# Optimization experiments

Measured on AMD Instinct MI355X. Metric: run time of the kernel, lower is better.

The kernel has to match this reference:

```python
import jax, jax.numpy as jnp
import numpy as np
from jax import lax

K = 15            # k_neighbors
EPS = 1e-8
N, D = 8192, 512


def _knn(emb, k):
    # pairwise euclidean distances via gram trick (torch.cdist p=2 equivalent)
    sq = jnp.sum(emb * emb, axis=1)                      # [N]
    d2 = sq[:, None] + sq[None, :] - 2.0 * (emb @ emb.T)  # [N, N]
    d = jnp.where(d2 > 0, jnp.sqrt(jnp.maximum(d2, 1e-24)), 0.0)
    neg_d, idx = lax.top_k(-d, k + 1)                    # smallest k+1 (incl. self)
    return -neg_d[:, 1:], idx[:, 1:]                     # drop self: [N,k], [N,k]


def _local_density(knn_dists):
    return 1.0 / (knn_dists.mean(axis=1) + EPS)          # [N]


def _angular_signature(emb, knn_idx, k):
    nb = emb[knn_idx]                                    # [N, k, D] gather
    v = nb - emb[:, None, :]                             # [N, k, D]
    v = v / jnp.maximum(jnp.linalg.norm(v, axis=2, keepdims=True), 1e-12)
    cos = jnp.einsum('nkd,nld->nkl', v, v)               # [N, k, k]
    iu0, iu1 = np.triu_indices(k, 1)                     # static upper-triangle mask
    return cos[:, iu0, iu1]                              # [N, k*(k-1)/2]


def setup_inputs() -> dict:
    key = jax.random.key(0)
    k1, k2 = jax.random.split(key)
    embeddings = jax.random.normal(k1, (N, D), dtype=jnp.float32)
    ref_embeddings = jax.random.normal(k2, (N, D), dtype=jnp.float32)
    return {"embeddings": embeddings, "ref_embeddings": ref_embeddings}


def reference(embeddings, ref_embeddings):
    k = K
    # reference geometry is a detached buffer (set_reference under no_grad)
    ref = lax.stop_gradient(ref_embeddings)
    ref_dists, ref_idx = _knn(ref, k)
    ref_density = _local_density(ref_dists)
    ref_angular = _angular_signature(ref, ref_idx, k)

    curr_dists, curr_idx = _knn(embeddings, k)

    # 1) normalized distance-distribution loss
    curr_dn = curr_dists / (curr_dists.mean(axis=1, keepdims=True) + EPS)
    ref_dn = ref_dists / (ref_dists.mean(axis=1, keepdims=True) + EPS)
    total = jnp.mean((curr_dn - ref_dn) ** 2)

    # 2) density preservation loss (use_density=True)
    curr_density = _local_density(curr_dists)
    cden = curr_density / (curr_density.mean() + EPS)
    rden = ref_density / (ref_density.mean() + EPS)
    total = total + 0.5 * jnp.mean((cden - rden) ** 2)

    # 3) angular structure loss (use_angular=True)
    curr_angular = _angular_signature(embeddings, curr_idx, k)
    total = total + 0.5 * jnp.mean((curr_angular - ref_angular) ** 2)
    return total
```

## Files before the change

kernel.cpp:

```cpp
#include <hip/hip_runtime.h>

#define N 8192
#define D 512
#define KNN 15
#define SC 8
#define NC 16
#define SPLITS 8
#define NCAND 32
#define NPAIR 105
#define EPSF 1e-8f

#define RB 32
#define CB 64
#define KB 32

#define INF __int_as_float(0x7f800000)

typedef __attribute__((ext_vector_type(4))) float f32x4;
typedef __attribute__((ext_vector_type(8))) short s16x8;
typedef __attribute__((ext_vector_type(8))) unsigned short u16x8;
typedef unsigned long long u64;

typedef const unsigned int __attribute__((address_space(1)))* gp_t;
typedef unsigned int __attribute__((address_space(3)))* lp_t;

__device__ __forceinline__ void gl_lds16(const void* g, void* l) {
  __builtin_amdgcn_global_load_lds((gp_t)g, (lp_t)l, 16, 0, 0);
}

__device__ __forceinline__ unsigned short bf16_rne(float x) {
  unsigned int u = __float_as_uint(x);
  return (unsigned short)((u + 0x7fffu + ((u >> 16) & 1u)) >> 16);
}

#define VMCNT4 asm volatile("s_waitcnt vmcnt(4)" ::: "memory")
#define VMCNT0 asm volatile("s_waitcnt vmcnt(0)" ::: "memory")
#define LGKM0  asm volatile("s_waitcnt lgkmcnt(0)" ::: "memory")
#define CFENCE asm volatile("" ::: "memory")

__global__ __launch_bounds__(256)
void k_sqnorm(const float* __restrict__ A, const float* __restrict__ B,
              float* __restrict__ sq)
{
  int tid = threadIdx.x;
  int lane = tid & 63;
  int row = blockIdx.x * 4 + (tid >> 6);
  const float* src = (row < N) ? (A + (size_t)row * D)
                               : (B + (size_t)(row - N) * D);
  const float4* s4 = (const float4*)src + lane * 2;
  float4 x0 = s4[0], x1 = s4[1];
  float s = x0.x*x0.x + x0.y*x0.y + x0.z*x0.z + x0.w*x0.w
          + x1.x*x1.x + x1.y*x1.y + x1.z*x1.z + x1.w*x1.w;
#pragma unroll
  for (int o = 32; o; o >>= 1) s += __shfl_xor(s, o);
  if (lane == 0) sq[row] = s;
}

__global__ __launch_bounds__(256)
void k_split_hi(const float* __restrict__ A, const float* __restrict__ B,
                unsigned short* __restrict__ hi)
{
  size_t t = (size_t)blockIdx.x * 256 + threadIdx.x;
  size_t base = t * 8;
  const float* src = (base < (size_t)N * D) ? (A + base) : (B + (base - (size_t)N * D));
  float4 x0 = ((const float4*)src)[0];
  float4 x1 = ((const float4*)src)[1];
  float xs[8] = {x0.x, x0.y, x0.z, x0.w, x1.x, x1.y, x1.z, x1.w};
  u16x8 hv;
#pragma unroll
  for (int j = 0; j < 8; ++j) hv[j] = bf16_rne(xs[j]);
  *(u16x8*)(hi + base) = hv;
}

__global__ __launch_bounds__(256, 4)
void k_knn1(const unsigned short* __restrict__ hi,
            const float* __restrict__ sqall,
            unsigned* __restrict__ pk)
{
  __shared__ __align__(16) char smem[40960];
  float* Dt = (float*)smem;
  unsigned* SK = (unsigned*)smem;

  const int tid = threadIdx.x;
  const int lane = tid & 63, w = tid >> 6;
  const int wr = w >> 1, wc = w & 1;
  const int fr = lane & 15, fq = lane >> 4;
  const int sgx = fq ^ ((fr >> 1) & 3);

  const int rb = blockIdx.x, split = blockIdx.y, which = blockIdx.z;
  const int row0 = rb * 128;
  const int c0 = split * 1024;
  const unsigned short* Hi = hi + (size_t)which * N * D;
  const float* sq = sqall + which * N;

  const int rr = tid >> 2, sseg = tid & 3;
  const int ssg = sseg ^ ((rr >> 1) & 3);
  const unsigned short* pAh = Hi + (size_t)(row0 + rr) * D + ssg * 8;
  const unsigned short* pBh = Hi + (size_t)(c0 + rr) * D + ssg * 8;

  auto stage = [&](int sel) {
    char* d = smem + (sel << 14) + (w << 10);
    gl_lds16(pAh, d);
    gl_lds16(pAh + 32768, d + 4096);
    gl_lds16(pBh, d + 8192);
    gl_lds16(pBh + 32768, d + 12288);
    pAh += 32; pBh += 32;
  };

  const int srow = tid >> 1, ssub = tid & 1;
  unsigned tv[SC];
#pragma unroll
  for (int j = 0; j < SC; ++j) tv[j] = 0xFFFFFFFFu;

  float sqr[4][4];
#pragma unroll
  for (int m = 0; m < 4; ++m)
#pragma unroll
    for (int j = 0; j < 4; ++j)
      sqr[m][j] = sq[row0 + wr * 64 + m * 16 + fq * 4 + j];

#pragma unroll 1
  for (int t = 0; t < 8; ++t) {
    const int ct = c0 + t * 128;
    float sqc[4];
#pragma unroll
    for (int n = 0; n < 4; ++n) sqc[n] = sq[ct + wc * 64 + n * 16 + fr];

    f32x4 acc[4][4];
#pragma unroll
    for (int m = 0; m < 4; ++m)
#pragma unroll
      for (int n = 0; n < 4; ++n) acc[m][n] = (f32x4){0.f, 0.f, 0.f, 0.f};

    stage(0);
    int cur = 0;
#pragma unroll 1
    for (int kt = 0; kt < 16; ++kt) {
      if (kt < 15) {
        stage(cur ^ 1);
        VMCNT4;
      } else {
        VMCNT0;
      }
      __builtin_amdgcn_s_barrier();
      CFENCE;

      const short* Sb = (const short*)(smem + (cur << 14));
      s16x8 ah[4], bh[4];
#pragma unroll
      for (int m = 0; m < 4; ++m)
        ah[m] = *(const s16x8*)(Sb + (wr * 64 + m * 16 + fr) * 32 + sgx * 8);
#pragma unroll
      for (int n = 0; n < 4; ++n)
        bh[n] = *(const s16x8*)(Sb + 4096 + (wc * 64 + n * 16 + fr) * 32 + sgx * 8);
#pragma unroll
      for (int m = 0; m < 4; ++m)
#pragma unroll
        for (int n = 0; n < 4; ++n)
          acc[m][n] = __builtin_amdgcn_mfma_f32_16x16x32_bf16(ah[m], bh[n], acc[m][n], 0, 0, 0);

      LGKM0;
      __builtin_amdgcn_s_barrier();
      CFENCE;
      cur ^= 1;
    }
    pAh -= 512; pBh += 65024;

#pragma unroll 1
    for (int h = 0; h < 2; ++h) {
      if (wc == h) {
#pragma unroll
        for (int m = 0; m < 4; ++m)
#pragma unroll
          for (int n = 0; n < 4; ++n) {
            const int cl = n * 16 + fr;
            const int gcol = ct + h * 64 + cl;
            const int rbase = wr * 64 + m * 16 + fq * 4;
#pragma unroll
            for (int j = 0; j < 4; ++j) {
              float d2 = fmaf(-2.0f, acc[m][n][j], sqr[m][j] + sqc[n]);
              if (row0 + rbase + j == gcol) d2 = INF;
              Dt[(rbase + j) * 68 + cl] = d2;
            }
          }
      }
      __syncthreads();
      {
        unsigned kth = tv[SC - 1];
        const int lb = t * 128 + h * 64 + ssub * 32;
#pragma unroll 1
        for (int g = 0; g < 8; ++g) {
          const f32x4 dv = *(const f32x4*)&Dt[srow * 68 + ssub * 32 + g * 4];
#pragma unroll
          for (int i = 0; i < 4; ++i) {
            const float d2c = fmaxf(dv[i], 0.0f);
            unsigned key = (__float_as_uint(d2c) & ~1023u) | (unsigned)(lb + g * 4 + i);
            if (key < kth) {
#pragma unroll
              for (int j = 0; j < SC; ++j) {
                const unsigned lo = min(tv[j], key);
                key = max(tv[j], key);
                tv[j] = lo;
              }
              kth = tv[SC - 1];
            }
          }
        }
      }
      __syncthreads();
    }
  }

#pragma unroll
  for (int j = 0; j < SC; ++j) SK[srow * 16 + ssub * 8 + j] = tv[j];
  __syncthreads();
  if (tid < 128) {
    const int grow = row0 + tid;
    const size_t pb = (((size_t)which * SPLITS + split) * N + grow) * NC;
    int p0 = 0, p1 = 0;
#pragma unroll
    for (int j = 0; j < NC; ++j) {
      const unsigned a = (p0 < SC) ? SK[tid * 16 + p0] : 0xFFFFFFFFu;
      const unsigned b = (p1 < SC) ? SK[tid * 16 + 8 + p1] : 0xFFFFFFFFu;
      const bool ta = a <= b;
      pk[pb + j] = ta ? a : b;
      if (ta) ++p0; else ++p1;
    }
  }
}

__global__ __launch_bounds__(256)
void k_cand(const unsigned* __restrict__ pk, int* __restrict__ cidx)
{
  const int flat = blockIdx.x * 256 + threadIdx.x;
  const int which = flat >> 13, row = flat & (N - 1);
  const size_t b0 = (((size_t)which * SPLITS + 0) * N + row) * NC;
  const size_t b1 = (((size_t)which * SPLITS + 1) * N + row) * NC;
  const size_t b2 = (((size_t)which * SPLITS + 2) * N + row) * NC;
  const size_t b3 = (((size_t)which * SPLITS + 3) * N + row) * NC;
  const size_t b4 = (((size_t)which * SPLITS + 4) * N + row) * NC;
  const size_t b5 = (((size_t)which * SPLITS + 5) * N + row) * NC;
  const size_t b6 = (((size_t)which * SPLITS + 6) * N + row) * NC;
  const size_t b7 = (((size_t)which * SPLITS + 7) * N + row) * NC;
  unsigned v0 = pk[b0], v1 = pk[b1], v2 = pk[b2], v3 = pk[b3];
  unsigned v4 = pk[b4], v5 = pk[b5], v6 = pk[b6], v7 = pk[b7];
  int p0 = 0, p1 = 0, p2 = 0, p3 = 0, p4 = 0, p5 = 0, p6 = 0, p7 = 0;
  const size_t ob = ((size_t)which * N + row) * NCAND;
#pragma unroll 1
  for (int j = 0; j < NCAND; ++j) {
    const bool a01 = v0 <= v1; const unsigned m01 = a01 ? v0 : v1; const int s01 = a01 ? 0 : 1;
    const bool a23 = v2 <= v3; const unsigned m23 = a23 ? v2 : v3; const int s23 = a23 ? 2 : 3;
    const bool a45 = v4 <= v5; const unsigned m45 = a45 ? v4 : v5; const int s45 = a45 ? 4 : 5;
    const bool a67 = v6 <= v7; const unsigned m67 = a67 ? v6 : v7; const int s67 = a67 ? 6 : 7;
    const bool qA = m01 <= m23; const unsigned mA = qA ? m01 : m23; const int sA = qA ? s01 : s23;
    const bool qB = m45 <= m67; const unsigned mB = qB ? m45 : m67; const int sB = qB ? s45 : s67;
    const bool qf = mA <= mB;  const unsigned m = qf ? mA : mB;    const int sw = qf ? sA : sB;
    cidx[ob + j] = (sw << 10) | (int)(m & 1023u);
    if      (sw == 0) { ++p0; v0 = (p0 < NC) ? pk[b0 + p0] : 0xFFFFFFFFu; }
    else if (sw == 1) { ++p1; v1 = (p1 < NC) ? pk[b1 + p1] : 0xFFFFFFFFu; }
    else if (sw == 2) { ++p2; v2 = (p2 < NC) ? pk[b2 + p2] : 0xFFFFFFFFu; }
    else if (sw == 3) { ++p3; v3 = (p3 < NC) ? pk[b3 + p3] : 0xFFFFFFFFu; }
    else if (sw == 4) { ++p4; v4 = (p4 < NC) ? pk[b4 + p4] : 0xFFFFFFFFu; }
    else if (sw == 5) { ++p5; v5 = (p5 < NC) ? pk[b5 + p5] : 0xFFFFFFFFu; }
    else if (sw == 6) { ++p6; v6 = (p6 < NC) ? pk[b6 + p6] : 0xFFFFFFFFu; }
    else              { ++p7; v7 = (p7 < NC) ? pk[b7 + p7] : 0xFFFFFFFFu; }
  }
}

__global__ __launch_bounds__(256)
void k_rescore(const float* __restrict__ emb, const float* __restrict__ ref,
               const float* __restrict__ sqall, const int* __restrict__ cidx,
               float* __restrict__ knnd, int* __restrict__ knni)
{
  const int tid = threadIdx.x;
  const int lane = tid & 63, w = tid >> 6;
  const int flat = blockIdx.x * 4 + w;
  const int which = flat >> 13, row = flat & (N - 1);
  const float* E = which ? ref : emb;
  const float* sq = sqall + which * N;
  const int* cb = cidx + ((size_t)which * N + row) * NCAND;

  const float4* orow = (const float4*)(E + (size_t)row * D) + lane * 2;
  const float4 o0 = orow[0], o1 = orow[1];
  const float sqr = sq[row];

  u64 mykey = ~0ull;
#pragma unroll 4
  for (int c = 0; c < NCAND; ++c) {
    const int cl = cb[c];
    const float4* crow = (const float4*)(E + (size_t)cl * D) + lane * 2;
    const float4 c0 = crow[0], c1 = crow[1];
    float s = o0.x*c0.x + o0.y*c0.y + o0.z*c0.z + o0.w*c0.w
            + o1.x*c1.x + o1.y*c1.y + o1.z*c1.z + o1.w*c1.w;
#pragma unroll
    for (int o = 32; o; o >>= 1) s += __shfl_xor(s, o);
    float d2 = fmaf(-2.0f, s, sqr + sq[cl]);
    d2 = fmaxf(d2, 0.0f);
    const u64 key = ((u64)__float_as_uint(d2) << 32) | (unsigned)cl;
    if (lane == c) mykey = key;
  }

#pragma unroll
  for (int k = 2; k <= 64; k <<= 1) {
#pragma unroll
    for (int j = k >> 1; j > 0; j >>= 1) {
      const u64 o = __shfl_xor(mykey, j);
      const bool up = ((lane & k) == 0);
      const bool lower = ((lane & j) == 0);
      const u64 mn = (mykey < o) ? mykey : o;
      const u64 mx = (mykey < o) ? o : mykey;
      mykey = (lower == up) ? mn : mx;
    }
  }

  const size_t ob = ((size_t)which * N + row) * KNN;
  if (lane < KNN) {
    const float d2v = __uint_as_float((unsigned)(mykey >> 32));
    knnd[ob + lane] = (d2v > 0.f) ? sqrtf(fmaxf(d2v, 1e-24f)) : 0.f;
    knni[ob + lane] = (int)(mykey & 0xffffffffu);
  }
}

__global__ __launch_bounds__(256)
void k_knn_fb(const float* __restrict__ Ecur, const float* __restrict__ Eref,
              const float* __restrict__ sqall,
              float* __restrict__ knnd, int* __restrict__ knni)
{
  const int which = blockIdx.y;
  const float* E = which ? Eref : Ecur;
  const float* sq = sqall + which * N;
  float* outd = knnd + (size_t)which * N * KNN;
  int* outi = knni + (size_t)which * N * KNN;
  const int row0 = blockIdx.x * RB;

  __shared__ float As[RB][KB + 1];
  __shared__ float Bs[KB][CB + 4];
  __shared__ float Dtf[RB][CB + 1];
  __shared__ float topv[RB][KNN];
  __shared__ int topi[RB][KNN];

  const int tid = threadIdx.x;
  const int tx = tid & 15, ty = tid >> 4;

  if (tid < RB) {
#pragma unroll
    for (int j = 0; j < KNN; ++j) { topv[tid][j] = INF; topi[tid][j] = -1; }
  }

  for (int ct = 0; ct < N; ct += CB) {
    float acc[2][4] = {{0.f,0.f,0.f,0.f},{0.f,0.f,0.f,0.f}};
    for (int kt = 0; kt < D; kt += KB) {
      __syncthreads();
      {
        int r = tid >> 3, c4 = (tid & 7) << 2;
        const float4 v = *(const float4*)&E[(size_t)(row0 + r) * D + kt + c4];
        As[r][c4+0] = v.x; As[r][c4+1] = v.y; As[r][c4+2] = v.z; As[r][c4+3] = v.w;
      }
      {
        int k = tid & 31, cbase = tid >> 5;
#pragma unroll
        for (int i = 0; i < 8; ++i) {
          int c = cbase + (i << 3);
          Bs[k][c] = E[(size_t)(ct + c) * D + kt + k];
        }
      }
      __syncthreads();
#pragma unroll
      for (int k = 0; k < KB; ++k) {
        float a0 = As[2*ty + 0][k], a1 = As[2*ty + 1][k];
        float4 b = *(const float4*)&Bs[k][tx << 2];
        acc[0][0] = fmaf(a0, b.x, acc[0][0]); acc[0][1] = fmaf(a0, b.y, acc[0][1]);
        acc[0][2] = fmaf(a0, b.z, acc[0][2]); acc[0][3] = fmaf(a0, b.w, acc[0][3]);
        acc[1][0] = fmaf(a1, b.x, acc[1][0]); acc[1][1] = fmaf(a1, b.y, acc[1][1]);
        acc[1][2] = fmaf(a1, b.z, acc[1][2]); acc[1][3] = fmaf(a1, b.w, acc[1][3]);
      }
    }
    {
      float sr0 = sq[row0 + 2*ty + 0], sr1 = sq[row0 + 2*ty + 1];
#pragma unroll
      for (int c = 0; c < 4; ++c) {
        int gc = ct + (tx << 2) + c;
        float scv = sq[gc];
        float d20 = sr0 + scv - 2.0f * acc[0][c];
        float d21 = sr1 + scv - 2.0f * acc[1][c];
        float d0 = (d20 > 0.0f) ? sqrtf(fmaxf(d20, 1e-24f)) : 0.0f;
        float d1 = (d21 > 0.0f) ? sqrtf(fmaxf(d21, 1e-24f)) : 0.0f;
        if (gc == row0 + 2*ty + 0) d0 = INF;
        if (gc == row0 + 2*ty + 1) d1 = INF;
        Dtf[2*ty + 0][(tx << 2) + c] = d0;
        Dtf[2*ty + 1][(tx << 2) + c] = d1;
      }
    }
    __syncthreads();
    if (tid < RB) {
      float kth = topv[tid][KNN-1];
      for (int c = 0; c < CB; ++c) {
        float d = Dtf[tid][c];
        if (d < kth) {
          int gi = ct + c;
          int j = KNN - 1;
          while (j > 0 && topv[tid][j-1] > d) {
            topv[tid][j] = topv[tid][j-1]; topi[tid][j] = topi[tid][j-1]; --j;
          }
          topv[tid][j] = d; topi[tid][j] = gi;
          kth = topv[tid][KNN-1];
        }
      }
    }
    __syncthreads();
  }
  if (tid < RB) {
    int gr = row0 + tid;
#pragma unroll
    for (int j = 0; j < KNN; ++j) {
      outd[(size_t)gr * KNN + j] = topv[tid][j];
      outi[(size_t)gr * KNN + j] = topi[tid][j];
    }
  }
}

__global__ __launch_bounds__(256)
void k_ang3(const float* __restrict__ Ecur, const float* __restrict__ Eref,
            const int* __restrict__ knni, float* __restrict__ angpart)
{
  __shared__ __align__(16) short Vb[16][520];
  __shared__ float Gp[4][256];
  __shared__ float G[256];
  __shared__ float invn[16];
  __shared__ float cref[NPAIR];
  __shared__ float red2[256];

  const int i = blockIdx.x;
  const int tid = threadIdx.x;
  const int lane = tid & 63;
  const int w = tid >> 6;
  const int base = lane * 8;

  float acc = 0.f;

#pragma unroll 1
  for (int pass = 0; pass < 2; ++pass) {
    const float* E = pass ? Ecur : Eref;
    const int* idx = knni + ((size_t)(pass ? 0 : 1) * N + i) * KNN;

    const float4* er = (const float4*)(E + (size_t)i * D) + lane * 2;
    const float4 e0 = er[0], e1 = er[1];

#pragma unroll 1
    for (int j = w; j < 16; j += 4) {
      u16x8 hv;
      if (j < 15) {
        const float* src = E + (size_t)idx[j] * D;
        const float4 x0 = *(const float4*)(src + base);
        const float4 x1 = *(const float4*)(src + base + 4);
        const float dd[8] = {x0.x-e0.x, x0.y-e0.y, x0.z-e0.z, x0.w-e0.w,
                             x1.x-e1.x, x1.y-e1.y, x1.z-e1.z, x1.w-e1.w};
#pragma unroll
        for (int q = 0; q < 8; ++q) hv[q] = bf16_rne(dd[q]);
      } else {
#pragma unroll
        for (int q = 0; q < 8; ++q) hv[q] = 0;
      }
      *(u16x8*)&Vb[j][base] = hv;
    }
    __syncthreads();

    {
      const int r = lane & 15, fq = lane >> 4;
      f32x4 g = (f32x4){0.f, 0.f, 0.f, 0.f};
#pragma unroll
      for (int s = 0; s < 4; ++s) {
        const s16x8 f = *(const s16x8*)&Vb[r][w * 128 + s * 32 + fq * 8];
        g = __builtin_amdgcn_mfma_f32_16x16x32_bf16(f, f, g, 0, 0, 0);
      }
#pragma unroll
      for (int r2 = 0; r2 < 4; ++r2)
        Gp[w][(fq * 4 + r2) * 16 + r] = g[r2];
    }
    __syncthreads();

    G[tid] = Gp[0][tid] + Gp[1][tid] + Gp[2][tid] + Gp[3][tid];
    __syncthreads();
    if (tid < 16) invn[tid] = 1.0f / fmaxf(sqrtf(G[tid * 17]), 1e-12f);
    __syncthreads();

    if (tid < NPAIR) {
      int a = 0, q = tid, rem = KNN - 1;
      while (q >= rem) { q -= rem; ++a; --rem; }
      const int b = a + 1 + q;
      const float cosv = G[a * 16 + b] * invn[a] * invn[b];
      if (pass == 0) cref[tid] = cosv;
      else { const float dd = cosv - cref[tid]; acc = dd * dd; }
    }
    __syncthreads();
  }

  red2[tid] = acc;
  __syncthreads();
  for (int o = 128; o; o >>= 1) {
    if (tid < o) red2[tid] += red2[tid + o];
    __syncthreads();
  }
  if (tid == 0) angpart[i] = red2[0];
}

__global__ __launch_bounds__(256)
void k_stats(const float* __restrict__ knnd, float* __restrict__ dens,
             float* __restrict__ loss1part)
{
  __shared__ float red[256];
  int n = blockIdx.x * 256 + threadIdx.x;
  const float* dc = knnd + (size_t)n * KNN;
  const float* dr = knnd + (size_t)(N + n) * KNN;
  float mc = 0.f, mr = 0.f;
#pragma unroll
  for (int j = 0; j < KNN; ++j) { mc += dc[j]; mr += dr[j]; }
  mc *= (1.0f / KNN); mr *= (1.0f / KNN);
  float ic = 1.0f / (mc + EPSF);
  float ir = 1.0f / (mr + EPSF);
  float s = 0.f;
#pragma unroll
  for (int j = 0; j < KNN; ++j) {
    float t = dc[j] * ic - dr[j] * ir;
    s = fmaf(t, t, s);
  }
  dens[n] = ic;
  dens[N + n] = ir;
  red[threadIdx.x] = s;
  __syncthreads();
  for (int o = 128; o; o >>= 1) {
    if (threadIdx.x < o) red[threadIdx.x] += red[threadIdx.x + o];
    __syncthreads();
  }
  if (threadIdx.x == 0) loss1part[blockIdx.x] = red[0];
}

__global__ __launch_bounds__(256)
void k_final(const float* __restrict__ loss1part, const float* __restrict__ dens,
             const float* __restrict__ angpart, float* __restrict__ out)
{
  __shared__ float red[256];
  const int t = threadIdx.x;

  float sc = 0.f, sr = 0.f;
  for (int n = t; n < N; n += 256) { sc += dens[n]; sr += dens[N + n]; }
  red[t] = sc; __syncthreads();
  for (int o = 128; o; o >>= 1) { if (t < o) red[t] += red[t + o]; __syncthreads(); }
  float scm = red[0]; __syncthreads();
  red[t] = sr; __syncthreads();
  for (int o = 128; o; o >>= 1) { if (t < o) red[t] += red[t + o]; __syncthreads(); }
  float srm = red[0]; __syncthreads();

  float icm = 1.0f / (scm / (float)N + EPSF);
  float irm = 1.0f / (srm / (float)N + EPSF);

  float l2 = 0.f;
  for (int n = t; n < N; n += 256) {
    float dd = dens[n] * icm - dens[N + n] * irm;
    l2 = fmaf(dd, dd, l2);
  }
  red[t] = l2; __syncthreads();
  for (int o = 128; o; o >>= 1) { if (t < o) red[t] += red[t + o]; __syncthreads(); }
  float l2sum = red[0]; __syncthreads();

  float l1 = (t < 32) ? loss1part[t] : 0.f;
  red[t] = l1; __syncthreads();
  for (int o = 128; o; o >>= 1) { if (t < o) red[t] += red[t + o]; __syncthreads(); }
  float l1sum = red[0]; __syncthreads();

  float l3 = 0.f;
  for (int n = t; n < N; n += 256) l3 += angpart[n];
  red[t] = l3; __syncthreads();
  for (int o = 128; o; o >>= 1) { if (t < o) red[t] += red[t + o]; __syncthreads(); }
  float l3sum = red[0];

  if (t == 0) {
    out[0] = l1sum / (float)(N * KNN)
           + 0.5f * l2sum / (float)N
           + 0.5f * l3sum / (float)(N * NPAIR);
  }
}

extern "C" void kernel_launch(void* const* d_in, const int* in_sizes, int n_in,
                              void* d_out, int out_size, void* d_ws, size_t ws_size,
                              hipStream_t stream)
{
  const float* emb = (const float*)d_in[0];
  const float* ref = (const float*)d_in[1];
  float* out = (float*)d_out;
  char* ws = (char*)d_ws;

  const size_t off_sq = 0;
  const size_t off_hi = off_sq + (size_t)2 * N * 4;

  const size_t m_off_pk   = off_hi + (size_t)2 * N * D * 2;
  const size_t m_off_cidx = m_off_pk + (size_t)2 * SPLITS * N * NC * 4;
  const size_t m_off_knnd = m_off_cidx + (size_t)2 * N * NCAND * 4;
  const size_t m_off_knni = m_off_knnd + (size_t)2 * N * KNN * 4;
  const size_t m_off_angp = m_off_knni + (size_t)2 * N * KNN * 4;
  const size_t m_off_dens = m_off_angp + (size_t)N * 4;
  const size_t m_off_l1   = m_off_dens + (size_t)2 * N * 4;
  const size_t NEED       = m_off_l1 + 4096;

  float* sq = (float*)(ws + off_sq);
  float* knnd; int* knni; float* angpart; float* dens; float* l1part;

  k_sqnorm<<<(2 * N) / 4, 256, 0, stream>>>(emb, ref, sq);

  if (ws_size >= NEED) {
    unsigned short* hi = (unsigned short*)(ws + off_hi);
    unsigned* pk = (unsigned*)(ws + m_off_pk);
    int* cidx = (int*)(ws + m_off_cidx);
    knnd = (float*)(ws + m_off_knnd);
    knni = (int*)(ws + m_off_knni);
    angpart = (float*)(ws + m_off_angp);
    dens = (float*)(ws + m_off_dens);
    l1part = (float*)(ws + m_off_l1);

    k_split_hi<<<(2 * N * D / 8) / 256, 256, 0, stream>>>(emb, ref, hi);
    k_knn1<<<dim3(N / 128, SPLITS, 2), 256, 0, stream>>>(hi, sq, pk);
    k_cand<<<(2 * N) / 256, 256, 0, stream>>>(pk, cidx);
    k_rescore<<<(2 * N) / 4, 256, 0, stream>>>(emb, ref, sq, cidx, knnd, knni);
  } else {
    size_t o = off_hi;
    knnd = (float*)(ws + o); o += (size_t)2 * N * KNN * 4;
    knni = (int*)(ws + o);   o += (size_t)2 * N * KNN * 4;
    angpart = (float*)(ws + o); o += (size_t)N * 4;
    dens = (float*)(ws + o); o += (size_t)2 * N * 4;
    l1part = (float*)(ws + o);
    k_knn_fb<<<dim3(N / RB, 2), 256, 0, stream>>>(emb, ref, sq, knnd, knni);
  }

  k_ang3<<<N, 256, 0, stream>>>(emb, ref, knni, angpart);
  k_stats<<<N / 256, 256, 0, stream>>>(knnd, dens, l1part);
  k_final<<<1, 256, 0, stream>>>(l1part, dens, angpart, out);
}
```

Measured before the change: 396.1 us.

## Fuse prep kernels and merge candidate selection, rescoring, stats into angular kernel

Merges the squared-norm and bf16 split kernels into one pass over the inputs. The candidate-merge, rescore, stats and angular kernels become a single per-row tail kernel that bitonic-sorts the 128 partial keys inside a wavefront, rescores, and uses the neighbours directly from shared memory. The knn tile kernel now packs full 13-bit column indices into the keys when writing to shared memory, which drops low mantissa bits used in candidate ordering. This removes several launches and the intermediate candidate, distance and index buffers, but only two of the four waves do the merge and rescore work in the tail, and the fallback path for small workspaces is gone.

New measurement: 367.2 us. 1.08x faster.

```diff
diff --git a/kernel.cpp b/kernel.cpp
--- a/kernel.cpp
+++ b/kernel.cpp
@@ -10,13 +10,10 @@
 #define NPAIR 105
 #define EPSF 1e-8f
 
-#define RB 32
-#define CB 64
-#define KB 32
-
 #define INF __int_as_float(0x7f800000)
 
 typedef __attribute__((ext_vector_type(4))) float f32x4;
+typedef __attribute__((ext_vector_type(4))) unsigned u32x4;
 typedef __attribute__((ext_vector_type(8))) short s16x8;
 typedef __attribute__((ext_vector_type(8))) unsigned short u16x8;
 typedef unsigned long long u64;
@@ -39,37 +36,28 @@
 #define CFENCE asm volatile("" ::: "memory")
 
 __global__ __launch_bounds__(256)
-void k_sqnorm(const float* __restrict__ A, const float* __restrict__ B,
-              float* __restrict__ sq)
+void k_prep(const float* __restrict__ A, const float* __restrict__ B,
+            unsigned short* __restrict__ hi, float* __restrict__ sq)
 {
-  int tid = threadIdx.x;
-  int lane = tid & 63;
-  int row = blockIdx.x * 4 + (tid >> 6);
+  const int tid = threadIdx.x;
+  const int lane = tid & 63;
+  const int row = blockIdx.x * 4 + (tid >> 6);
   const float* src = (row < N) ? (A + (size_t)row * D)
                                : (B + (size_t)(row - N) * D);
   const float4* s4 = (const float4*)src + lane * 2;
-  float4 x0 = s4[0], x1 = s4[1];
-  float s = x0.x*x0.x + x0.y*x0.y + x0.z*x0.z + x0.w*x0.w
-          + x1.x*x1.x + x1.y*x1.y + x1.z*x1.z + x1.w*x1.w;
+  const float4 x0 = s4[0], x1 = s4[1];
+  const float xs[8] = {x0.x, x0.y, x0.z, x0.w, x1.x, x1.y, x1.z, x1.w};
+  u16x8 hv;
+  float s = 0.f;
+#pragma unroll
+  for (int j = 0; j < 8; ++j) {
+    hv[j] = bf16_rne(xs[j]);
+    s = fmaf(xs[j], xs[j], s);
+  }
+  *(u16x8*)(hi + (size_t)row * D + lane * 8) = hv;
 #pragma unroll
   for (int o = 32; o; o >>= 1) s += __shfl_xor(s, o);
   if (lane == 0) sq[row] = s;
-}
-
-__global__ __launch_bounds__(256)
-void k_split_hi(const float* __restrict__ A, const float* __restrict__ B,
-                unsigned short* __restrict__ hi)
-{
-  size_t t = (size_t)blockIdx.x * 256 + threadIdx.x;
-  size_t base = t * 8;
-  const float* src = (base < (size_t)N * D) ? (A + base) : (B + (base - (size_t)N * D));
-  float4 x0 = ((const float4*)src)[0];
-  float4 x1 = ((const float4*)src)[1];
-  float xs[8] = {x0.x, x0.y, x0.z, x0.w, x1.x, x1.y, x1.z, x1.w};
-  u16x8 hv;
-#pragma unroll
-  for (int j = 0; j < 8; ++j) hv[j] = bf16_rne(xs[j]);
-  *(u16x8*)(hi + base) = hv;
 }
 
 __global__ __launch_bounds__(256, 4)
@@ -78,7 +66,7 @@
             unsigned* __restrict__ pk)
 {
   __shared__ __align__(16) char smem[40960];
-  float* Dt = (float*)smem;
+  unsigned* DtU = (unsigned*)smem;
   unsigned* SK = (unsigned*)smem;
 
   const int tid = threadIdx.x;
@@ -178,23 +166,22 @@
             const int rbase = wr * 64 + m * 16 + fq * 4;
 #pragma unroll
             for (int j = 0; j < 4; ++j) {
-              float d2 = fmaf(-2.0f, acc[m][n][j], sqr[m][j] + sqc[n]);
-              if (row0 + rbase + j == gcol) d2 = INF;
-              Dt[(rbase + j) * 68 + cl] = d2;
+              const float d2 = fmaf(-2.0f, acc[m][n][j], sqr[m][j] + sqc[n]);
+              unsigned key = (__float_as_uint(fmaxf(d2, 0.f)) & ~8191u) | (unsigned)gcol;
+              if (row0 + rbase + j == gcol) key = 0xFFFFFFFFu;
+              DtU[(rbase + j) * 68 + cl] = key;
             }
           }
       }
       __syncthreads();
       {
         unsigned kth = tv[SC - 1];
-        const int lb = t * 128 + h * 64 + ssub * 32;
 #pragma unroll 1
         for (int g = 0; g < 8; ++g) {
-          const f32x4 dv = *(const f32x4*)&Dt[srow * 68 + ssub * 32 + g * 4];
+          const u32x4 dv = *(const u32x4*)&DtU[srow * 68 + ssub * 32 + g * 4];
 #pragma unroll
           for (int i = 0; i < 4; ++i) {
-            const float d2c = fmaxf(dv[i], 0.0f);
-            unsigned key = (__float_as_uint(d2c) & ~1023u) | (unsigned)(lb + g * 4 + i);
+            unsigned key = dv[i];
             if (key < kth) {
 #pragma unroll
               for (int j = 0; j < SC; ++j) {
@@ -230,198 +217,10 @@
 }
 
 __global__ __launch_bounds__(256)
-void k_cand(const unsigned* __restrict__ pk, int* __restrict__ cidx)
-{
-  const int flat = blockIdx.x * 256 + threadIdx.x;
-  const int which = flat >> 13, row = flat & (N - 1);
-  const size_t b0 = (((size_t)which * SPLITS + 0) * N + row) * NC;
-  const size_t b1 = (((size_t)which * SPLITS + 1) * N + row) * NC;
-  const size_t b2 = (((size_t)which * SPLITS + 2) * N + row) * NC;
-  const size_t b3 = (((size_t)which * SPLITS + 3) * N + row) * NC;
-  const size_t b4 = (((size_t)which * SPLITS + 4) * N + row) * NC;
-  const size_t b5 = (((size_t)which * SPLITS + 5) * N + row) * NC;
-  const size_t b6 = (((size_t)which * SPLITS + 6) * N + row) * NC;
-  const size_t b7 = (((size_t)which * SPLITS + 7) * N + row) * NC;
-  unsigned v0 = pk[b0], v1 = pk[b1], v2 = pk[b2], v3 = pk[b3];
-  unsigned v4 = pk[b4], v5 = pk[b5], v6 = pk[b6], v7 = pk[b7];
-  int p0 = 0, p1 = 0, p2 = 0, p3 = 0, p4 = 0, p5 = 0, p6 = 0, p7 = 0;
-  const size_t ob = ((size_t)which * N + row) * NCAND;
-#pragma unroll 1
-  for (int j = 0; j < NCAND; ++j) {
-    const bool a01 = v0 <= v1; const unsigned m01 = a01 ? v0 : v1; const int s01 = a01 ? 0 : 1;
-    const bool a23 = v2 <= v3; const unsigned m23 = a23 ? v2 : v3; const int s23 = a23 ? 2 : 3;
-    const bool a45 = v4 <= v5; const unsigned m45 = a45 ? v4 : v5; const int s45 = a45 ? 4 : 5;
-    const bool a67 = v6 <= v7; const unsigned m67 = a67 ? v6 : v7; const int s67 = a67 ? 6 : 7;
-    const bool qA = m01 <= m23; const unsigned mA = qA ? m01 : m23; const int sA = qA ? s01 : s23;
-    const bool qB = m45 <= m67; const unsigned mB = qB ? m45 : m67; const int sB = qB ? s45 : s67;
-    const bool qf = mA <= mB;  const unsigned m = qf ? mA : mB;    const int sw = qf ? sA : sB;
-    cidx[ob + j] = (sw << 10) | (int)(m & 1023u);
-    if      (sw == 0) { ++p0; v0 = (p0 < NC) ? pk[b0 + p0] : 0xFFFFFFFFu; }
-    else if (sw == 1) { ++p1; v1 = (p1 < NC) ? pk[b1 + p1] : 0xFFFFFFFFu; }
-    else if (sw == 2) { ++p2; v2 = (p2 < NC) ? pk[b2 + p2] : 0xFFFFFFFFu; }
-    else if (sw == 3) { ++p3; v3 = (p3 < NC) ? pk[b3 + p3] : 0xFFFFFFFFu; }
-    else if (sw == 4) { ++p4; v4 = (p4 < NC) ? pk[b4 + p4] : 0xFFFFFFFFu; }
-    else if (sw == 5) { ++p5; v5 = (p5 < NC) ? pk[b5 + p5] : 0xFFFFFFFFu; }
-    else if (sw == 6) { ++p6; v6 = (p6 < NC) ? pk[b6 + p6] : 0xFFFFFFFFu; }
-    else              { ++p7; v7 = (p7 < NC) ? pk[b7 + p7] : 0xFFFFFFFFu; }
-  }
-}
-
-__global__ __launch_bounds__(256)
-void k_rescore(const float* __restrict__ emb, const float* __restrict__ ref,
-               const float* __restrict__ sqall, const int* __restrict__ cidx,
-               float* __restrict__ knnd, int* __restrict__ knni)
-{
-  const int tid = threadIdx.x;
-  const int lane = tid & 63, w = tid >> 6;
-  const int flat = blockIdx.x * 4 + w;
-  const int which = flat >> 13, row = flat & (N - 1);
-  const float* E = which ? ref : emb;
-  const float* sq = sqall + which * N;
-  const int* cb = cidx + ((size_t)which * N + row) * NCAND;
-
-  const float4* orow = (const float4*)(E + (size_t)row * D) + lane * 2;
-  const float4 o0 = orow[0], o1 = orow[1];
-  const float sqr = sq[row];
-
-  u64 mykey = ~0ull;
-#pragma unroll 4
-  for (int c = 0; c < NCAND; ++c) {
-    const int cl = cb[c];
-    const float4* crow = (const float4*)(E + (size_t)cl * D) + lane * 2;
-    const float4 c0 = crow[0], c1 = crow[1];
-    float s = o0.x*c0.x + o0.y*c0.y + o0.z*c0.z + o0.w*c0.w
-            + o1.x*c1.x + o1.y*c1.y + o1.z*c1.z + o1.w*c1.w;
-#pragma unroll
-    for (int o = 32; o; o >>= 1) s += __shfl_xor(s, o);
-    float d2 = fmaf(-2.0f, s, sqr + sq[cl]);
-    d2 = fmaxf(d2, 0.0f);
-    const u64 key = ((u64)__float_as_uint(d2) << 32) | (unsigned)cl;
-    if (lane == c) mykey = key;
-  }
-
-#pragma unroll
-  for (int k = 2; k <= 64; k <<= 1) {
-#pragma unroll
-    for (int j = k >> 1; j > 0; j >>= 1) {
-      const u64 o = __shfl_xor(mykey, j);
-      const bool up = ((lane & k) == 0);
-      const bool lower = ((lane & j) == 0);
-      const u64 mn = (mykey < o) ? mykey : o;
-      const u64 mx = (mykey < o) ? o : mykey;
-      mykey = (lower == up) ? mn : mx;
-    }
-  }
-
-  const size_t ob = ((size_t)which * N + row) * KNN;
-  if (lane < KNN) {
-    const float d2v = __uint_as_float((unsigned)(mykey >> 32));
-    knnd[ob + lane] = (d2v > 0.f) ? sqrtf(fmaxf(d2v, 1e-24f)) : 0.f;
-    knni[ob + lane] = (int)(mykey & 0xffffffffu);
-  }
-}
-
-__global__ __launch_bounds__(256)
-void k_knn_fb(const float* __restrict__ Ecur, const float* __restrict__ Eref,
-              const float* __restrict__ sqall,
-              float* __restrict__ knnd, int* __restrict__ knni)
-{
-  const int which = blockIdx.y;
-  const float* E = which ? Eref : Ecur;
-  const float* sq = sqall + which * N;
-  float* outd = knnd + (size_t)which * N * KNN;
-  int* outi = knni + (size_t)which * N * KNN;
-  const int row0 = blockIdx.x * RB;
-
-  __shared__ float As[RB][KB + 1];
-  __shared__ float Bs[KB][CB + 4];
-  __shared__ float Dtf[RB][CB + 1];
-  __shared__ float topv[RB][KNN];
-  __shared__ int topi[RB][KNN];
-
-  const int tid = threadIdx.x;
-  const int tx = tid & 15, ty = tid >> 4;
-
-  if (tid < RB) {
-#pragma unroll
-    for (int j = 0; j < KNN; ++j) { topv[tid][j] = INF; topi[tid][j] = -1; }
-  }
-
-  for (int ct = 0; ct < N; ct += CB) {
-    float acc[2][4] = {{0.f,0.f,0.f,0.f},{0.f,0.f,0.f,0.f}};
-    for (int kt = 0; kt < D; kt += KB) {
-      __syncthreads();
-      {
-        int r = tid >> 3, c4 = (tid & 7) << 2;
-        const float4 v = *(const float4*)&E[(size_t)(row0 + r) * D + kt + c4];
-        As[r][c4+0] = v.x; As[r][c4+1] = v.y; As[r][c4+2] = v.z; As[r][c4+3] = v.w;
-      }
-      {
-        int k = tid & 31, cbase = tid >> 5;
-#pragma unroll
-        for (int i = 0; i < 8; ++i) {
-          int c = cbase + (i << 3);
-          Bs[k][c] = E[(size_t)(ct + c) * D + kt + k];
-        }
-      }
-      __syncthreads();
-#pragma unroll
-      for (int k = 0; k < KB; ++k) {
-        float a0 = As[2*ty + 0][k], a1 = As[2*ty + 1][k];
-        float4 b = *(const float4*)&Bs[k][tx << 2];
-        acc[0][0] = fmaf(a0, b.x, acc[0][0]); acc[0][1] = fmaf(a0, b.y, acc[0][1]);
-        acc[0][2] = fmaf(a0, b.z, acc[0][2]); acc[0][3] = fmaf(a0, b.w, acc[0][3]);
-        acc[1][0] = fmaf(a1, b.x, acc[1][0]); acc[1][1] = fmaf(a1, b.y, acc[1][1]);
-        acc[1][2] = fmaf(a1, b.z, acc[1][2]); acc[1][3] = fmaf(a1, b.w, acc[1][3]);
-      }
-    }
-    {
-      float sr0 = sq[row0 + 2*ty + 0], sr1 = sq[row0 + 2*ty + 1];
-#pragma unroll
-      for (int c = 0; c < 4; ++c) {
-        int gc = ct + (tx << 2) + c;
-        float scv = sq[gc];
-        float d20 = sr0 + scv - 2.0f * acc[0][c];
-        float d21 = sr1 + scv - 2.0f * acc[1][c];
-        float d0 = (d20 > 0.0f) ? sqrtf(fmaxf(d20, 1e-24f)) : 0.0f;
-        float d1 = (d21 > 0.0f) ? sqrtf(fmaxf(d21, 1e-24f)) : 0.0f;
-        if (gc == row0 + 2*ty + 0) d0 = INF;
-        if (gc == row0 + 2*ty + 1) d1 = INF;
-        Dtf[2*ty + 0][(tx << 2) + c] = d0;
-        Dtf[2*ty + 1][(tx << 2) + c] = d1;
-      }
-    }
-    __syncthreads();
-    if (tid < RB) {
-      float kth = topv[tid][KNN-1];
-      for (int c = 0; c < CB; ++c) {
-        float d = Dtf[tid][c];
-        if (d < kth) {
-          int gi = ct + c;
-          int j = KNN - 1;
-          while (j > 0 && topv[tid][j-1] > d) {
-            topv[tid][j] = topv[tid][j-1]; topi[tid][j] = topi[tid][j-1]; --j;
-          }
-          topv[tid][j] = d; topi[tid][j] = gi;
-          kth = topv[tid][KNN-1];
-        }
-      }
-    }
-    __syncthreads();
-  }
-  if (tid < RB) {
-    int gr = row0 + tid;
-#pragma unroll
-    for (int j = 0; j < KNN; ++j) {
-      outd[(size_t)gr * KNN + j] = topv[tid][j];
-      outi[(size_t)gr * KNN + j] = topi[tid][j];
-    }
-  }
-}
-
-__global__ __launch_bounds__(256)
-void k_ang3(const float* __restrict__ Ecur, const float* __restrict__ Eref,
-            const int* __restrict__ knni, float* __restrict__ angpart)
+void k_tail(const float* __restrict__ emb, const float* __restrict__ ref,
+            const float* __restrict__ sqall, const unsigned* __restrict__ pk,
+            float* __restrict__ dens, float* __restrict__ l1p,
+            float* __restrict__ angp)
 {
   __shared__ __align__(16) short Vb[16][520];
   __shared__ float Gp[4][256];
@@ -429,19 +228,111 @@
   __shared__ float invn[16];
   __shared__ float cref[NPAIR];
   __shared__ float red2[256];
+  __shared__ int idxs[2][16];
+  __shared__ float dls[2][16];
 
   const int i = blockIdx.x;
   const int tid = threadIdx.x;
   const int lane = tid & 63;
   const int w = tid >> 6;
+
+  if (w < 2) {
+    const int which = 1 - w;
+    const float* E = which ? ref : emb;
+    const float* sqm = sqall + which * N;
+
+    const int sp = lane >> 3, jj = lane & 7;
+    const size_t kb = (((size_t)which * SPLITS + sp) * N + i) * NC;
+    unsigned v0 = pk[kb + jj];
+    unsigned v1 = pk[kb + 8 + jj];
+
+#pragma unroll
+    for (int k = 2; k <= 128; k <<= 1) {
+#pragma unroll
+      for (int s = k >> 1; s > 0; s >>= 1) {
+        if (s == 64) {
+          const unsigned mn = min(v0, v1), mx = max(v0, v1);
+          v0 = mn; v1 = mx;
+        } else {
+          const unsigned o0 = __shfl_xor(v0, s);
+          const unsigned o1 = __shfl_xor(v1, s);
+          const bool low = ((lane & s) == 0);
+          const bool dir0 = ((lane & k) == 0);
+          const bool dir1 = (((64 + lane) & k) == 0);
+          const unsigned a0 = min(v0, o0), b0 = max(v0, o0);
+          v0 = (low == dir0) ? a0 : b0;
+          const unsigned a1 = min(v1, o1), b1 = max(v1, o1);
+          v1 = (low == dir1) ? a1 : b1;
+        }
+      }
+    }
+
+    const float4* orow = (const float4*)(E + (size_t)i * D) + lane * 2;
+    const float4 o0 = orow[0], o1 = orow[1];
+    const float sqr_ = sqm[i];
+
+    u64 mykey = ~0ull;
+#pragma unroll 4
+    for (int c = 0; c < NCAND; ++c) {
+      const int cl = (int)(__shfl(v0, c) & 8191u);
+      const float4* crow = (const float4*)(E + (size_t)cl * D) + lane * 2;
+      const float4 c0 = crow[0], c1 = crow[1];
+      float s = o0.x*c0.x + o0.y*c0.y + o0.z*c0.z + o0.w*c0.w
+              + o1.x*c1.x + o1.y*c1.y + o1.z*c1.z + o1.w*c1.w;
+#pragma unroll
+      for (int o = 32; o; o >>= 1) s += __shfl_xor(s, o);
+      float d2 = fmaf(-2.0f, s, sqr_ + sqm[cl]);
+      d2 = fmaxf(d2, 0.0f);
+      const u64 key = ((u64)__float_as_uint(d2) << 32) | (unsigned)cl;
+      if (lane == c) mykey = key;
+    }
+
+#pragma unroll
+    for (int k = 2; k <= 64; k <<= 1) {
+#pragma unroll
+      for (int j = k >> 1; j > 0; j >>= 1) {
+        const u64 o = __shfl_xor(mykey, j);
+        const bool up = ((lane & k) == 0);
+        const bool lower = ((lane & j) == 0);
+        const u64 mn = (mykey < o) ? mykey : o;
+        const u64 mx = (mykey < o) ? o : mykey;
+        mykey = (lower == up) ? mn : mx;
+      }
+    }
+
+    if (lane < KNN) {
+      const float d2v = __uint_as_float((unsigned)(mykey >> 32));
+      dls[w][lane] = (d2v > 0.f) ? sqrtf(fmaxf(d2v, 1e-24f)) : 0.f;
+      idxs[w][lane] = (int)(mykey & 0xffffffffu);
+    }
+  }
+  __syncthreads();
+
+  if (tid == 0) {
+    float mr = 0.f, mc = 0.f;
+#pragma unroll
+    for (int j = 0; j < KNN; ++j) { mr += dls[0][j]; mc += dls[1][j]; }
+    mr *= (1.0f / KNN); mc *= (1.0f / KNN);
+    const float ir = 1.0f / (mr + EPSF);
+    const float ic = 1.0f / (mc + EPSF);
+    float s1 = 0.f;
+#pragma unroll
+    for (int j = 0; j < KNN; ++j) {
+      const float t = dls[1][j] * ic - dls[0][j] * ir;
+      s1 = fmaf(t, t, s1);
+    }
+    dens[i] = ic;
+    dens[N + i] = ir;
+    l1p[i] = s1;
+  }
+  __syncthreads();
+
   const int base = lane * 8;
-
   float acc = 0.f;
 
 #pragma unroll 1
   for (int pass = 0; pass < 2; ++pass) {
-    const float* E = pass ? Ecur : Eref;
-    const int* idx = knni + ((size_t)(pass ? 0 : 1) * N + i) * KNN;
+    const float* E = pass ? emb : ref;
 
     const float4* er = (const float4*)(E + (size_t)i * D) + lane * 2;
     const float4 e0 = er[0], e1 = er[1];
@@ -450,7 +341,7 @@
     for (int j = w; j < 16; j += 4) {
       u16x8 hv;
       if (j < 15) {
-        const float* src = E + (size_t)idx[j] * D;
+        const float* src = E + (size_t)idxs[pass][j] * D;
         const float4 x0 = *(const float4*)(src + base);
         const float4 x1 = *(const float4*)(src + base + 4);
         const float dd[8] = {x0.x-e0.x, x0.y-e0.y, x0.z-e0.z, x0.w-e0.w,
@@ -501,43 +392,12 @@
     if (tid < o) red2[tid] += red2[tid + o];
     __syncthreads();
   }
-  if (tid == 0) angpart[i] = red2[0];
+  if (tid == 0) angp[i] = red2[0];
 }
 
 __global__ __launch_bounds__(256)
-void k_stats(const float* __restrict__ knnd, float* __restrict__ dens,
-             float* __restrict__ loss1part)
-{
-  __shared__ float red[256];
-  int n = blockIdx.x * 256 + threadIdx.x;
-  const float* dc = knnd + (size_t)n * KNN;
-  const float* dr = knnd + (size_t)(N + n) * KNN;
-  float mc = 0.f, mr = 0.f;
-#pragma unroll
-  for (int j = 0; j < KNN; ++j) { mc += dc[j]; mr += dr[j]; }
-  mc *= (1.0f / KNN); mr *= (1.0f / KNN);
-  float ic = 1.0f / (mc + EPSF);
-  float ir = 1.0f / (mr + EPSF);
-  float s = 0.f;
-#pragma unroll
-  for (int j = 0; j < KNN; ++j) {
-    float t = dc[j] * ic - dr[j] * ir;
-    s = fmaf(t, t, s);
-  }
-  dens[n] = ic;
-  dens[N + n] = ir;
-  red[threadIdx.x] = s;
-  __syncthreads();
-  for (int o = 128; o; o >>= 1) {
-    if (threadIdx.x < o) red[threadIdx.x] += red[threadIdx.x + o];
-    __syncthreads();
-  }
-  if (threadIdx.x == 0) loss1part[blockIdx.x] = red[0];
-}
-
-__global__ __launch_bounds__(256)
-void k_final(const float* __restrict__ loss1part, const float* __restrict__ dens,
-             const float* __restrict__ angpart, float* __restrict__ out)
+void k_final(const float* __restrict__ l1p, const float* __restrict__ dens,
+             const float* __restrict__ angp, float* __restrict__ out)
 {
   __shared__ float red[256];
   const int t = threadIdx.x;
@@ -551,28 +411,29 @@
   for (int o = 128; o; o >>= 1) { if (t < o) red[t] += red[t + o]; __syncthreads(); }
   float srm = red[0]; __syncthreads();
 
-  float icm = 1.0f / (scm / (float)N + EPSF);
-  float irm = 1.0f / (srm / (float)N + EPSF);
+  const float icm = 1.0f / (scm / (float)N + EPSF);
+  const float irm = 1.0f / (srm / (float)N + EPSF);
 
   float l2 = 0.f;
   for (int n = t; n < N; n += 256) {
-    float dd = dens[n] * icm - dens[N + n] * irm;
+    const float dd = dens[n] * icm - dens[N + n] * irm;
     l2 = fmaf(dd, dd, l2);
   }
   red[t] = l2; __syncthreads();
   for (int o = 128; o; o >>= 1) { if (t < o) red[t] += red[t + o]; __syncthreads(); }
-  float l2sum = red[0]; __syncthreads();
-
-  float l1 = (t < 32) ? loss1part[t] : 0.f;
+  const float l2sum = red[0]; __syncthreads();
+
+  float l1 = 0.f;
+  for (int n = t; n < N; n += 256) l1 += l1p[n];
   red[t] = l1; __syncthreads();
   for (int o = 128; o; o >>= 1) { if (t < o) red[t] += red[t + o]; __syncthreads(); }
-  float l1sum = red[0]; __syncthreads();
+  const float l1sum = red[0]; __syncthreads();
 
   float l3 = 0.f;
-  for (int n = t; n < N; n += 256) l3 += angpart[n];
+  for (int n = t; n < N; n += 256) l3 += angp[n];
   red[t] = l3; __syncthreads();
   for (int o = 128; o; o >>= 1) { if (t < o) red[t] += red[t + o]; __syncthreads(); }
-  float l3sum = red[0];
+  const float l3sum = red[0];
 
   if (t == 0) {
     out[0] = l1sum / (float)(N * KNN)
@@ -590,48 +451,22 @@
   float* out = (float*)d_out;
   char* ws = (char*)d_ws;
 
-  const size_t off_sq = 0;
-  const size_t off_hi = off_sq + (size_t)2 * N * 4;
-
-  const size_t m_off_pk   = off_hi + (size_t)2 * N * D * 2;
-  const size_t m_off_cidx = m_off_pk + (size_t)2 * SPLITS * N * NC * 4;
-  const size_t m_off_knnd = m_off_cidx + (size_t)2 * N * NCAND * 4;
-  const size_t m_off_knni = m_off_knnd + (size_t)2 * N * KNN * 4;
-  const size_t m_off_angp = m_off_knni + (size_t)2 * N * KNN * 4;
-  const size_t m_off_dens = m_off_angp + (size_t)N * 4;
-  const size_t m_off_l1   = m_off_dens + (size_t)2 * N * 4;
-  const size_t NEED       = m_off_l1 + 4096;
+  const size_t off_sq   = 0;
+  const size_t off_hi   = off_sq + (size_t)2 * N * 4;
+  const size_t off_pk   = off_hi + (size_t)2 * N * D * 2;
+  const size_t off_dens = off_pk + (size_t)2 * SPLITS * N * NC * 4;
+  const size_t off_l1   = off_dens + (size_t)2 * N * 4;
+  const size_t off_ang  = off_l1 + (size_t)N * 4;
 
   float* sq = (float*)(ws + off_sq);
-  float* knnd; int* knni; float* angpart; float* dens; float* l1part;
-
-  k_sqnorm<<<(2 * N) / 4, 256, 0, stream>>>(emb, ref, sq);
-
-  if (ws_size >= NEED) {
-    unsigned short* hi = (unsigned short*)(ws + off_hi);
-    unsigned* pk = (unsigned*)(ws + m_off_pk);
-    int* cidx = (int*)(ws + m_off_cidx);
-    knnd = (float*)(ws + m_off_knnd);
-    knni = (int*)(ws + m_off_knni);
-    angpart = (float*)(ws + m_off_angp);
-    dens = (float*)(ws + m_off_dens);
-    l1part = (float*)(ws + m_off_l1);
-
-    k_split_hi<<<(2 * N * D / 8) / 256, 256, 0, stream>>>(emb, ref, hi);
-    k_knn1<<<dim3(N / 128, SPLITS, 2), 256, 0, stream>>>(hi, sq, pk);
-    k_cand<<<(2 * N) / 256, 256, 0, stream>>>(pk, cidx);
-    k_rescore<<<(2 * N) / 4, 256, 0, stream>>>(emb, ref, sq, cidx, knnd, knni);
-  } else {
-    size_t o = off_hi;
-    knnd = (float*)(ws + o); o += (size_t)2 * N * KNN * 4;
-    knni = (int*)(ws + o);   o += (size_t)2 * N * KNN * 4;
-    angpart = (float*)(ws + o); o += (size_t)N * 4;
-    dens = (float*)(ws + o); o += (size_t)2 * N * 4;
-    l1part = (float*)(ws + o);
-    k_knn_fb<<<dim3(N / RB, 2), 256, 0, stream>>>(emb, ref, sq, knnd, knni);
-  }
-
-  k_ang3<<<N, 256, 0, stream>>>(emb, ref, knni, angpart);
-  k_stats<<<N / 256, 256, 0, stream>>>(knnd, dens, l1part);
-  k_final<<<1, 256, 0, stream>>>(l1part, dens, angpart, out);
-}
+  unsigned short* hi = (unsigned short*)(ws + off_hi);
+  unsigned* pk = (unsigned*)(ws + off_pk);
+  float* dens = (float*)(ws + off_dens);
+  float* l1p = (float*)(ws + off_l1);
+  float* angp = (float*)(ws + off_ang);
+
+  k_prep<<<(2 * N) / 4, 256, 0, stream>>>(emb, ref, hi, sq);
+  k_knn1<<<dim3(N / 128, SPLITS, 2), 256, 0, stream>>>(hi, sq, pk);
+  k_tail<<<N, 256, 0, stream>>>(emb, ref, sq, pk, dens, l1p, angp);
+  k_final<<<1, 256, 0, stream>>>(l1p, dens, angp, out);
+}
```
